# Optimization experiments

Measured on AMD Instinct MI355X. Metric: run time of the kernel, lower is better.

Reference implementation:

```python
import jax, jax.numpy as jnp
import numpy as np

B, S, D = 4, 1024, 1024
H, HD = 16, 64
MAXPOS = 1024  # max_position_embeddings


def setup_inputs() -> dict:
    key = jax.random.key(0)
    ks = jax.random.split(key, 10)
    sc = 0.02
    return {
        "hidden_states": jax.random.normal(ks[0], (B, S, D), dtype=jnp.float32),
        "attention_mask": jnp.zeros((B, 1, 1, S), dtype=jnp.float32),
        "across_attention_prior": jax.random.uniform(ks[1], (B, H, S, S), dtype=jnp.float32),
        "head_mask": jnp.ones((1, H, 1, 1), dtype=jnp.float32),
        "Wq": jax.random.normal(ks[2], (D, D), dtype=jnp.float32) * sc,
        "bq": jnp.zeros((D,), dtype=jnp.float32),
        "Wk": jax.random.normal(ks[3], (D, D), dtype=jnp.float32) * sc,
        "bk": jnp.zeros((D,), dtype=jnp.float32),
        "Wv": jax.random.normal(ks[4], (D, D), dtype=jnp.float32) * sc,
        "bv": jnp.zeros((D,), dtype=jnp.float32),
        "dist_emb": jax.random.normal(ks[5], (2 * MAXPOS - 1, HD), dtype=jnp.float32) * sc,
    }


def _heads(x):
    # [B,S,D] -> [B,H,S,HD]
    return x.reshape(B, S, H, HD).transpose(0, 2, 1, 3)


def reference(hidden_states, attention_mask, across_attention_prior, head_mask,
              Wq, bq, Wk, bk, Wv, bv, dist_emb):
    q = _heads(hidden_states @ Wq + bq)  # [B,H,S,HD]
    k = _heads(hidden_states @ Wk + bk)
    v = _heads(hidden_states @ Wv + bv)

    scores = jnp.einsum("bhld,bhrd->bhlr", q, k)

    # relative_key_query positional bias
    pos = jnp.arange(S)
    distance = pos[:, None] - pos[None, :]  # [S,S]
    pe = dist_emb[distance + MAXPOS - 1]  # [S,S,HD] (l, r, d)
    scores = scores + jnp.einsum("bhld,lrd->bhlr", q, pe)
    scores = scores + jnp.einsum("bhrd,lrd->bhlr", k, pe)

    scores = scores / jnp.sqrt(jnp.float32(HD))
    scores = scores + attention_mask  # additive mask, broadcast [B,1,1,S]

    probs = jax.nn.softmax(scores, axis=-1)
    probs = probs * across_attention_prior  # post-softmax multiplicative prior
    probs = probs * head_mask  # dropout prob = 0 (eval)

    ctx = jnp.einsum("bhlr,bhrd->bhld", probs, v)
    ctx = ctx.transpose(0, 2, 1, 3).reshape(B, S, D)
    return ctx
```

## Files before the change

kernel.cpp:

```cpp
#include <hip/hip_runtime.h>


typedef unsigned short u16;
typedef unsigned int   u32;
typedef __attribute__((ext_vector_type(8))) short bfx8;
typedef __attribute__((ext_vector_type(4))) float f32x4;
typedef __attribute__((ext_vector_type(4))) unsigned short u16x4;

#define MFMA_BF16(a, b, c) __builtin_amdgcn_mfma_f32_16x16x32_bf16(a, b, c, 0, 0, 0)

__device__ __forceinline__ u16 f2bf(float f) {
    union { float f; u32 u; } c; c.f = f;
    u32 u = c.u;
    return (u16)((u + 0x7FFFu + ((u >> 16) & 1u)) >> 16);
}
__device__ __forceinline__ float bf2f(u16 v) {
    union { u32 u; float f; } c; c.u = ((u32)v) << 16;
    return c.f;
}
__device__ __forceinline__ float load_f(const void* p, long i, bool bf) {
    return bf ? bf2f(((const u16*)p)[i]) : ((const float*)p)[i];
}

__device__ __forceinline__ void gload16(const u16* g, u16* l) {
    __builtin_amdgcn_global_load_lds(
        (__attribute__((address_space(1))) void*)g,
        (__attribute__((address_space(3))) void*)l, 16, 0, 0);
}

__device__ __forceinline__ void wg_barrier() {
    asm volatile("s_waitcnt lgkmcnt(0)" ::: "memory");
    __builtin_amdgcn_s_barrier();
    asm volatile("" ::: "memory");
}

__global__ void k_detect(const u32* hid, int* flags) {
    __shared__ int cnt;
    if (threadIdx.x == 0) cnt = 0;
    __syncthreads();
    int c = 0;
    for (int i = threadIdx.x; i < 1024; i += 256) {
        u32 w = hid[i];
        u32 e = (w >> 7) & 0xFFu;
        if (e >= 100u && e <= 140u) c++;
    }
    atomicAdd(&cnt, c);
    __syncthreads();
    if (threadIdx.x == 0) flags[0] = (cnt > 512) ? 1 : 0;
}

__global__ void k_prep(const void* hidden, const void* dist, const void* mask,
                       const void* hm, const void* bq, const void* bk,
                       const void* bv, const int* flags, u16* hid_bf,
                       u16* dist_bf, float* mask_f, float* hm_f, float* bias_f) {
    const bool bf = flags[0] != 0;
    const long tid = (long)blockIdx.x * 256 + threadIdx.x;

    if (bf) {
        ((int4*)hid_bf)[tid] = ((const int4*)hidden)[tid];
    } else {
        const float* hf = (const float*)hidden + tid * 8;
        int4 o; u16* op = (u16*)&o;
#pragma unroll
        for (int j = 0; j < 8; j++) op[j] = f2bf(hf[j]);
        ((int4*)hid_bf)[tid] = o;
    }
    if (tid < 16376) {
        if (bf) {
            ((int4*)dist_bf)[tid] = ((const int4*)dist)[tid];
        } else {
            const float* df = (const float*)dist + tid * 8;
            int4 o; u16* op = (u16*)&o;
#pragma unroll
            for (int j = 0; j < 8; j++) op[j] = f2bf(df[j]);
            ((int4*)dist_bf)[tid] = o;
        }
    }
    if (tid < 4096) mask_f[tid] = load_f(mask, tid, bf);
    if (tid < 3072) {
        const void* src = (tid < 1024) ? bq : ((tid < 2048) ? bk : bv);
        bias_f[tid] = load_f(src, tid & 1023, bf);
    }
    if (tid < 16) hm_f[tid] = load_f(hm, tid, bf);
}

__global__ void k_transpose(const void* Wq, const void* Wk, const void* Wv,
                            const int* flags, u16* wt) {
    const bool bf = flags[0] != 0;
    __shared__ float t[32][33];
    const int z = blockIdx.z;
    const void* W = (z == 0) ? Wq : ((z == 1) ? Wk : Wv);
    int x = blockIdx.x * 32 + threadIdx.x;
    for (int i = 0; i < 4; i++) {
        int y = blockIdx.y * 32 + threadIdx.y + i * 8;
        t[threadIdx.y + i * 8][threadIdx.x] = load_f(W, (long)y * 1024 + x, bf);
    }
    __syncthreads();
    int x2 = blockIdx.y * 32 + threadIdx.x;
    u16* out = wt + (long)z * 1024 * 1024;
    for (int i = 0; i < 4; i++) {
        int y2 = blockIdx.x * 32 + threadIdx.y + i * 8;
        out[(long)y2 * 1024 + x2] = f2bf(t[threadIdx.x][threadIdx.y + i * 8]);
    }
}

__global__ __launch_bounds__(256, 3)
void k_qkv_gemm(const u16* A, const u16* Bt, const float* bias,
                u16* qb, u16* kb, u16* vb) {
    __shared__ u16 sA[128 * 64];
    __shared__ u16 sB[128 * 64];
    const int tid = threadIdx.x;
    const int w = tid >> 6, lane = tid & 63;
    const int quad = lane >> 4, nl = lane & 15;
    const int wr = w >> 1, wc = w & 1;
    const int bid0 = blockIdx.y * 24 + blockIdx.x;
    const int bid = (bid0 & 7) * 96 + (bid0 >> 3);
    const int n0 = (bid % 24) * 128, m0 = (bid / 24) * 128;

    f32x4 acc[4][4];
#pragma unroll
    for (int a = 0; a < 4; a++)
#pragma unroll
        for (int b = 0; b < 4; b++) acc[a][b] = (f32x4){0.f, 0.f, 0.f, 0.f};

    const int srow = 32 * w + (lane >> 3);
    const int seg = lane & 7;

    for (int kt = 0; kt < 16; kt++) {
        const int k0 = kt * 64;
        __syncthreads();
#pragma unroll
        for (int j = 0; j < 4; j++) {
            int row = srow + 8 * j;
            int ss = (seg ^ (row & 7)) * 8;
            gload16(A + (long)(m0 + row) * 1024 + k0 + ss, sA + (32 * w + 8 * j) * 64);
            gload16(Bt + (long)(n0 + row) * 1024 + k0 + ss, sB + (32 * w + 8 * j) * 64);
        }
        __syncthreads();

#pragma unroll
        for (int hh = 0; hh < 2; hh++) {
            bfx8 af[4], bfr[4];
#pragma unroll
            for (int f = 0; f < 4; f++) {
                int Ra = 64 * wr + 16 * f + nl;
                int Rb = 64 * wc + 16 * f + nl;
                af[f]  = *(const bfx8*)(sA + Ra * 64 + (((4 * hh + quad) ^ (Ra & 7)) * 8));
                bfr[f] = *(const bfx8*)(sB + Rb * 64 + (((4 * hh + quad) ^ (Rb & 7)) * 8));
            }
#pragma unroll
            for (int fm = 0; fm < 4; fm++)
#pragma unroll
                for (int fn = 0; fn < 4; fn++)
                    acc[fm][fn] = MFMA_BF16(af[fm], bfr[fn], acc[fm][fn]);
        }
    }

#pragma unroll
    for (int fm = 0; fm < 4; fm++) {
#pragma unroll
        for (int fn = 0; fn < 4; fn++) {
            int n = n0 + 64 * wc + 16 * fn + nl;
            int which = n >> 10, hcol = n & 1023;
            int h = hcol >> 6, hd = hcol & 63;
            u16* op = (which == 0) ? qb : ((which == 1) ? kb : vb);
            float bias_v = bias[n];
#pragma unroll
            for (int reg = 0; reg < 4; reg++) {
                int m = m0 + 64 * wr + 16 * fm + 4 * quad + reg;
                int b = m >> 10, s = m & 1023;
                float v = acc[fm][fn][reg] + bias_v;
                op[((long)((b * 16 + h) * 1024 + s)) * 64 + hd] = f2bf(v);
            }
        }
    }
}

__global__ __launch_bounds__(512, 4)
void k_attn(const u16* qb, const u16* kb, const u16* vb, const u16* Eb,
            const float* maskf, const float* hmf, const void* prior,
            const int* flags, void* out) {
    constexpr int PT = 72;
    constexpr int PD = 132;
    constexpr int PX = 66;
    __shared__ __align__(16) char smem[79872];
    u16* sQ  = (u16*)(smem);
    u16* sK  = (u16*)(smem + 9216);
    u16* sVT = (u16*)(smem + 18432);
    u16* sE  = (u16*)(smem + 27648);
    u16* sP  = (u16*)(smem + 27648);
    u16* sDq = (u16*)(smem + 46080);
    u16* sDk = (u16*)(smem + 62976);
    float* accx = (float*)(smem + 46080);
    float* zs   = (float*)(smem + 9216);

    const int tid = threadIdx.x;
    const int W = tid >> 6, lane = tid & 63;
    const int s = W >> 1, c = W & 1;
    const int quad = lane >> 4, nl = lane & 15;
    const int bh = blockIdx.x, b = bh >> 4, h = bh & 15;
    const int l0 = blockIdx.y * 64;
    const bool bf = flags[0] != 0;

    const u16* qbh = qb + (long)bh * 65536;
    const u16* kbh = kb + (long)bh * 65536;
    const u16* vbh = vb + (long)bh * 65536;

    {
        int row = tid >> 3, s8 = tid & 7;
        *(int4*)(sQ + row * PT + s8 * 8) = *(const int4*)(qbh + (l0 + row) * 64 + s8 * 8);
    }

    const int erow = tid >> 3, es8 = tid & 7;
    const int jb_base = l0 + 960;

    int4 nK0, nE0, nE1, nV0;
    {
        nK0 = *(const int4*)(kbh + erow * 64 + es8 * 8);
        int j0 = jb_base + erow;       if (j0 > 2046) j0 = 2046;
        int j1 = jb_base + 64 + erow;  if (j1 > 2046) j1 = 2046;
        nE0 = *(const int4*)(Eb + (long)j0 * 64 + es8 * 8);
        nE1 = *(const int4*)(Eb + (long)j1 * 64 + es8 * 8);
        nV0 = *(const int4*)(vbh + lane * 64 + W * 8);
    }

    wg_barrier();
    const bfx8 aq0 = *(const bfx8*)(sQ + (16 * s + nl) * PT + quad * 8);
    const bfx8 aq1 = *(const bfx8*)(sQ + (16 * s + nl) * PT + quad * 8 + 32);

    const int dql = c ? s + 3 : s,     dqh = c ? s + 4 : s + 2;
    const int dkl = c ? 6 - s : 3 - s, dkh = c ? 7 - s : 5 - s;

    f32x4 accv[4];
#pragma unroll
    for (int f = 0; f < 4; f++) accv[f] = (f32x4){0.f, 0.f, 0.f, 0.f};
    float zrow = 0.f;

    for (int it = 0; it < 16; it++) {
        const int r0 = it * 64;
        wg_barrier();

        *(int4*)(sK + erow * PT + es8 * 8)        = nK0;
        *(int4*)(sE + erow * PT + es8 * 8)        = nE0;
        *(int4*)(sE + (64 + erow) * PT + es8 * 8) = nE1;
        {
            const u16* pv = (const u16*)&nV0;
#pragma unroll
            for (int j2 = 0; j2 < 8; j2++) sVT[(W * 8 + j2) * PT + lane] = pv[j2];
        }

        f32x4 mvec[2], prv[2];
#pragma unroll
        for (int f2 = 0; f2 < 2; f2++) {
            const int colr = r0 + 32 * c + 16 * f2 + 4 * quad;
            mvec[f2] = *(const f32x4*)(maskf + b * 1024 + colr);
            long prow = ((long)(bh * 1024 + l0 + 16 * s + nl)) * 1024 + colr;
            if (bf) {
                u16x4 t = *(const u16x4*)((const u16*)prior + prow);
                prv[f2] = (f32x4){bf2f(t[0]), bf2f(t[1]), bf2f(t[2]), bf2f(t[3])};
            } else {
                prv[f2] = *(const f32x4*)((const float*)prior + prow);
            }
        }

        if (it < 15) {
            const int r0n = r0 + 64;
            const int jbn = jb_base - r0n;
            nK0 = *(const int4*)(kbh + (r0n + erow) * 64 + es8 * 8);
            int j0 = jbn + erow;       if (j0 > 2046) j0 = 2046;
            int j1 = jbn + 64 + erow;  if (j1 > 2046) j1 = 2046;
            nE0 = *(const int4*)(Eb + (long)j0 * 64 + es8 * 8);
            nE1 = *(const int4*)(Eb + (long)j1 * 64 + es8 * 8);
            nV0 = *(const int4*)(vbh + (r0n + lane) * 64 + W * 8);
        }
        wg_barrier();

        const bfx8 ak0 = *(const bfx8*)(sK + (16 * s + nl) * PT + quad * 8);
        const bfx8 ak1 = *(const bfx8*)(sK + (16 * s + nl) * PT + quad * 8 + 32);

#pragma unroll
        for (int fc = 0; fc < 8; fc++) {
            const bool uq = (fc >= dql) && (fc <= dqh);
            const bool uk = (fc >= dkl) && (fc <= dkh);
            if (!(uq || uk)) continue;
            const int ub = fc * 16;
            const int R = ub + nl;
            bfx8 be0 = *(const bfx8*)(sE + R * PT + quad * 8);
            bfx8 be1 = *(const bfx8*)(sE + R * PT + quad * 8 + 32);
            if (uq) {
                f32x4 dq = (f32x4){0.f, 0.f, 0.f, 0.f};
                dq = MFMA_BF16(be0, aq0, dq);
                dq = MFMA_BF16(be1, aq1, dq);
                u16x4 dqp;
#pragma unroll
                for (int reg = 0; reg < 4; reg++) dqp[reg] = f2bf(dq[reg]);
                *(u16x4*)(sDq + (16 * s + nl) * PD + ub + 4 * quad) = dqp;
            }
            if (uk) {
                f32x4 dk = (f32x4){0.f, 0.f, 0.f, 0.f};
                dk = MFMA_BF16(ak0, be0, dk);
                dk = MFMA_BF16(ak1, be1, dk);
#pragma unroll
                for (int reg = 0; reg < 4; reg++)
                    sDk[(16 * s + 4 * quad + reg) * PD + ub + nl] = f2bf(dk[reg]);
            }
        }
        f32x4 accs[2];
#pragma unroll
        for (int f2 = 0; f2 < 2; f2++) {
            const int R = (2 * c + f2) * 16 + nl;
            bfx8 ka0 = *(const bfx8*)(sK + R * PT + quad * 8);
            bfx8 ka1 = *(const bfx8*)(sK + R * PT + quad * 8 + 32);
            f32x4 sv = (f32x4){0.f, 0.f, 0.f, 0.f};
            sv = MFMA_BF16(ka0, aq0, sv);
            sv = MFMA_BF16(ka1, aq1, sv);
            accs[f2] = sv;
        }
        wg_barrier();

        u16x4 pw4[2];
        const int li = 16 * s + nl;
#pragma unroll
        for (int f2 = 0; f2 < 2; f2++) {
#pragma unroll
            for (int reg = 0; reg < 4; reg++) {
                int ri = (2 * c + f2) * 16 + 4 * quad + reg;
                int u = li - ri + 63;
                float sv = (accs[f2][reg] + bf2f(sDq[li * PD + u])
                            + bf2f(sDk[ri * PD + u])) * 0.125f + mvec[f2][reg];
                float e = __expf(sv);
                zrow += e;
                pw4[f2][reg] = f2bf(e * prv[f2][reg]);
            }
        }

#pragma unroll
        for (int f2 = 0; f2 < 2; f2++)
            *(u16x4*)(sP + li * PT + 32 * c + 16 * f2 + 4 * quad) = pw4[f2];

        const bfx8 ap = *(const bfx8*)(sP + li * PT + 32 * c + quad * 8);
#pragma unroll
        for (int fd = 0; fd < 4; fd++) {
            bfx8 bv = *(const bfx8*)(sVT + (fd * 16 + nl) * PT + 32 * c + quad * 8);
            accv[fd] = MFMA_BF16(ap, bv, accv[fd]);
        }
    }

    zrow += __shfl_xor(zrow, 16);
    zrow += __shfl_xor(zrow, 32);

    wg_barrier();
    if (c == 1) {
#pragma unroll
        for (int fd = 0; fd < 4; fd++)
#pragma unroll
            for (int reg = 0; reg < 4; reg++)
                accx[(16 * s + 4 * quad + reg) * PX + fd * 16 + nl] = accv[fd][reg];
    }
    if (quad == 0) zs[(16 * s + nl) * 2 + c] = zrow;
    wg_barrier();
    if (c == 0) {
        const float hm = hmf[h];
        float zt[4];
#pragma unroll
        for (int reg = 0; reg < 4; reg++) {
            int li2 = 16 * s + 4 * quad + reg;
            zt[reg] = zs[li2 * 2] + zs[li2 * 2 + 1];
        }
#pragma unroll
        for (int fd = 0; fd < 4; fd++) {
#pragma unroll
            for (int reg = 0; reg < 4; reg++) {
                int li2 = 16 * s + 4 * quad + reg;
                int d = fd * 16 + nl;
                float val = (accv[fd][reg] + accx[li2 * PX + fd * 16 + nl]) * hm / zt[reg];
                long oidx = ((long)(b * 1024 + l0 + li2)) * 1024 + h * 64 + d;
                if (bf) ((u16*)out)[oidx] = f2bf(val);
                else    ((float*)out)[oidx] = val;
            }
        }
    }
}

extern "C" void kernel_launch(void* const* d_in, const int* in_sizes, int n_in,
                              void* d_out, int out_size, void* d_ws, size_t ws_size,
                              hipStream_t stream) {
    char* ws = (char*)d_ws;
    int*   flags   = (int*)ws;
    u16*   hid_bf  = (u16*)(ws + 256);
    u16*   wt_bf   = (u16*)(ws + 8388864);
    u16*   dist_bf = (u16*)(ws + 14680320);
    float* mask_f  = (float*)(ws + 14942464);
    float* bias_f  = (float*)(ws + 14958848);
    float* hm_f    = (float*)(ws + 14971136);
    u16*   q_bf    = (u16*)(ws + 14971392);
    u16*   k_bf    = (u16*)(ws + 23360000);
    u16*   v_bf    = (u16*)(ws + 31748608);

    k_detect<<<1, 256, 0, stream>>>((const u32*)d_in[0], flags);
    k_prep<<<2048, 256, 0, stream>>>(d_in[0], d_in[10], d_in[1], d_in[3],
                                     d_in[5], d_in[7], d_in[9], flags,
                                     hid_bf, dist_bf, mask_f, hm_f, bias_f);
    k_transpose<<<dim3(32, 32, 3), dim3(32, 8), 0, stream>>>(
        d_in[4], d_in[6], d_in[8], flags, wt_bf);
    k_qkv_gemm<<<dim3(24, 32), 256, 0, stream>>>(hid_bf, wt_bf, bias_f,
                                                 q_bf, k_bf, v_bf);
    k_attn<<<dim3(64, 16), 512, 0, stream>>>(q_bf, k_bf, v_bf, dist_bf,
                                             mask_f, hm_f, d_in[2], flags, d_out);
}
```

Measured before the change: 499.8 us.

## Emit V pre-transposed from QKV GEMM and double-buffer V tiles via direct-to-LDS loads

The QKV GEMM epilogue now stages the V block in shared memory and writes V transposed as [b,h,d,s], so the attention kernel no longer transposes V with scalar LDS stores each iteration. The attention kernel loads V tiles with gload16 into two swizzled LDS buffers, prefetching the next tile while the current one is used. It also swaps the MFMA operand order for the Dk bias so the result can be stored as packed u16x4 instead of scattered scalar writes. In exchange the GEMM epilogue gains an extra sync and LDS round-trip for V blocks, and the LDS layout in the attention kernel is reshuffled.

```diff
diff --git a/kernel.cpp b/kernel.cpp
--- a/kernel.cpp
+++ b/kernel.cpp
@@ -106,9 +106,10 @@
 
 __global__ __launch_bounds__(256, 3)
 void k_qkv_gemm(const u16* A, const u16* Bt, const float* bias,
-                u16* qb, u16* kb, u16* vb) {
-    __shared__ u16 sA[128 * 64];
-    __shared__ u16 sB[128 * 64];
+                u16* qb, u16* kb, u16* vt) {
+    __shared__ u16 smemg[128 * 64 * 2];
+    u16* sA = smemg;
+    u16* sB = smemg + 128 * 64;
     const int tid = threadIdx.x;
     const int w = tid >> 6, lane = tid & 63;
     const int quad = lane >> 4, nl = lane & 15;
@@ -156,42 +157,72 @@
         }
     }
 
-#pragma unroll
-    for (int fm = 0; fm < 4; fm++) {
-#pragma unroll
-        for (int fn = 0; fn < 4; fn++) {
-            int n = n0 + 64 * wc + 16 * fn + nl;
-            int which = n >> 10, hcol = n & 1023;
-            int h = hcol >> 6, hd = hcol & 63;
-            u16* op = (which == 0) ? qb : ((which == 1) ? kb : vb);
-            float bias_v = bias[n];
-#pragma unroll
-            for (int reg = 0; reg < 4; reg++) {
-                int m = m0 + 64 * wr + 16 * fm + 4 * quad + reg;
-                int b = m >> 10, s = m & 1023;
-                float v = acc[fm][fn][reg] + bias_v;
-                op[((long)((b * 16 + h) * 1024 + s)) * 64 + hd] = f2bf(v);
-            }
+    if (n0 < 2048) {
+#pragma unroll
+        for (int fm = 0; fm < 4; fm++) {
+#pragma unroll
+            for (int fn = 0; fn < 4; fn++) {
+                int n = n0 + 64 * wc + 16 * fn + nl;
+                int which = n >> 10, hcol = n & 1023;
+                int h = hcol >> 6, hd = hcol & 63;
+                u16* op = (which == 0) ? qb : kb;
+                float bias_v = bias[n];
+#pragma unroll
+                for (int reg = 0; reg < 4; reg++) {
+                    int m = m0 + 64 * wr + 16 * fm + 4 * quad + reg;
+                    int b = m >> 10, s = m & 1023;
+                    float v = acc[fm][fn][reg] + bias_v;
+                    op[((long)((b * 16 + h) * 1024 + s)) * 64 + hd] = f2bf(v);
+                }
+            }
+        }
+    } else {
+        __syncthreads();
+        u16* t = smemg;
+#pragma unroll
+        for (int fm = 0; fm < 4; fm++) {
+#pragma unroll
+            for (int fn = 0; fn < 4; fn++) {
+                int row = 64 * wc + 16 * fn + nl;
+                float bias_v = bias[n0 + row];
+                u16x4 pack;
+#pragma unroll
+                for (int reg = 0; reg < 4; reg++)
+                    pack[reg] = f2bf(acc[fm][fn][reg] + bias_v);
+                int unit = (8 * wr + 2 * fm + (quad >> 1)) ^ (row & 7);
+                *(u16x4*)((char*)t + row * 256 + unit * 16 + (quad & 1) * 8) = pack;
+            }
+        }
+        __syncthreads();
+        const int row = tid >> 1, u0 = (tid & 1) * 8;
+        const int d = row & 63, hloc = row >> 6;
+        const int h = ((n0 & 1023) >> 6) + hloc;
+        const int b = m0 >> 10, s0 = m0 & 1023;
+        u16* dst = vt + (((long)((b * 16 + h) * 64 + d)) << 10) + s0;
+#pragma unroll
+        for (int k = 0; k < 8; k++) {
+            *(int4*)(dst + (u0 + k) * 8) = *(const int4*)(t + row * 128 + (u0 + k) * 8);
         }
     }
 }
 
 __global__ __launch_bounds__(512, 4)
-void k_attn(const u16* qb, const u16* kb, const u16* vb, const u16* Eb,
+void k_attn(const u16* qb, const u16* kb, const u16* vt, const u16* Eb,
             const float* maskf, const float* hmf, const void* prior,
             const int* flags, void* out) {
     constexpr int PT = 72;
     constexpr int PD = 132;
     constexpr int PX = 66;
-    __shared__ __align__(16) char smem[79872];
-    u16* sQ  = (u16*)(smem);
-    u16* sK  = (u16*)(smem + 9216);
-    u16* sVT = (u16*)(smem + 18432);
-    u16* sE  = (u16*)(smem + 27648);
-    u16* sP  = (u16*)(smem + 27648);
-    u16* sDq = (u16*)(smem + 46080);
-    u16* sDk = (u16*)(smem + 62976);
-    float* accx = (float*)(smem + 46080);
+    __shared__ __align__(16) char smem[78848];
+    u16* sVT1 = (u16*)(smem);
+    u16* sQ   = (u16*)(smem);
+    u16* sK   = (u16*)(smem + 9216);
+    u16* sVT0 = (u16*)(smem + 18432);
+    u16* sE   = (u16*)(smem + 26624);
+    u16* sP   = (u16*)(smem + 26624);
+    u16* sDq  = (u16*)(smem + 45056);
+    u16* sDk  = (u16*)(smem + 61952);
+    float* accx = (float*)(smem + 45056);
     float* zs   = (float*)(smem + 9216);
 
     const int tid = threadIdx.x;
@@ -204,7 +235,11 @@
 
     const u16* qbh = qb + (long)bh * 65536;
     const u16* kbh = kb + (long)bh * 65536;
-    const u16* vbh = vb + (long)bh * 65536;
+    const u16* vtp = vt + (long)bh * 65536;
+
+    const int vd = 8 * W + (lane >> 3), vk = lane & 7;
+
+    gload16(vtp + (long)vd * 1024 + 0 + vk * 8, sVT0 + 512 * W);
 
     {
         int row = tid >> 3, s8 = tid & 7;
@@ -214,14 +249,13 @@
     const int erow = tid >> 3, es8 = tid & 7;
     const int jb_base = l0 + 960;
 
-    int4 nK0, nE0, nE1, nV0;
+    int4 nK0, nE0, nE1;
     {
         nK0 = *(const int4*)(kbh + erow * 64 + es8 * 8);
         int j0 = jb_base + erow;       if (j0 > 2046) j0 = 2046;
         int j1 = jb_base + 64 + erow;  if (j1 > 2046) j1 = 2046;
         nE0 = *(const int4*)(Eb + (long)j0 * 64 + es8 * 8);
         nE1 = *(const int4*)(Eb + (long)j1 * 64 + es8 * 8);
-        nV0 = *(const int4*)(vbh + lane * 64 + W * 8);
     }
 
     wg_barrier();
@@ -243,11 +277,6 @@
         *(int4*)(sK + erow * PT + es8 * 8)        = nK0;
         *(int4*)(sE + erow * PT + es8 * 8)        = nE0;
         *(int4*)(sE + (64 + erow) * PT + es8 * 8) = nE1;
-        {
-            const u16* pv = (const u16*)&nV0;
-#pragma unroll
-            for (int j2 = 0; j2 < 8; j2++) sVT[(W * 8 + j2) * PT + lane] = pv[j2];
-        }
 
         f32x4 mvec[2], prv[2];
 #pragma unroll
@@ -271,9 +300,13 @@
             int j1 = jbn + 64 + erow;  if (j1 > 2046) j1 = 2046;
             nE0 = *(const int4*)(Eb + (long)j0 * 64 + es8 * 8);
             nE1 = *(const int4*)(Eb + (long)j1 * 64 + es8 * 8);
-            nV0 = *(const int4*)(vbh + (r0n + lane) * 64 + W * 8);
         }
         wg_barrier();
+
+        if (it < 15) {
+            u16* vbuf_n = ((it + 1) & 1) ? sVT1 : sVT0;
+            gload16(vtp + (long)vd * 1024 + (r0 + 64) + vk * 8, vbuf_n + 512 * W);
+        }
 
         const bfx8 ak0 = *(const bfx8*)(sK + (16 * s + nl) * PT + quad * 8);
         const bfx8 ak1 = *(const bfx8*)(sK + (16 * s + nl) * PT + quad * 8 + 32);
@@ -298,11 +331,12 @@
             }
             if (uk) {
                 f32x4 dk = (f32x4){0.f, 0.f, 0.f, 0.f};
-                dk = MFMA_BF16(ak0, be0, dk);
-                dk = MFMA_BF16(ak1, be1, dk);
-#pragma unroll
-                for (int reg = 0; reg < 4; reg++)
-                    sDk[(16 * s + 4 * quad + reg) * PD + ub + nl] = f2bf(dk[reg]);
+                dk = MFMA_BF16(be0, ak0, dk);
+                dk = MFMA_BF16(be1, ak1, dk);
+                u16x4 dkp;
+#pragma unroll
+                for (int reg = 0; reg < 4; reg++) dkp[reg] = f2bf(dk[reg]);
+                *(u16x4*)(sDk + (16 * s + nl) * PD + ub + 4 * quad) = dkp;
             }
         }
         f32x4 accs[2];
@@ -338,10 +372,12 @@
         for (int f2 = 0; f2 < 2; f2++)
             *(u16x4*)(sP + li * PT + 32 * c + 16 * f2 + 4 * quad) = pw4[f2];
 
+        const u16* vbuf = (it & 1) ? sVT1 : sVT0;
         const bfx8 ap = *(const bfx8*)(sP + li * PT + 32 * c + quad * 8);
 #pragma unroll
         for (int fd = 0; fd < 4; fd++) {
-            bfx8 bv = *(const bfx8*)(sVT + (fd * 16 + nl) * PT + 32 * c + quad * 8);
+            const int R = fd * 16 + nl;
+            bfx8 bv = *(const bfx8*)(vbuf + R * 64 + (((4 * c + quad) ^ (R & 7)) * 8));
             accv[fd] = MFMA_BF16(ap, bv, accv[fd]);
         }
     }
@@ -395,7 +431,7 @@
     float* hm_f    = (float*)(ws + 14971136);
     u16*   q_bf    = (u16*)(ws + 14971392);
     u16*   k_bf    = (u16*)(ws + 23360000);
-    u16*   v_bf    = (u16*)(ws + 31748608);
+    u16*   vt_bf   = (u16*)(ws + 31748608);
 
     k_detect<<<1, 256, 0, stream>>>((const u32*)d_in[0], flags);
     k_prep<<<2048, 256, 0, stream>>>(d_in[0], d_in[10], d_in[1], d_in[3],
@@ -404,7 +440,7 @@
     k_transpose<<<dim3(32, 32, 3), dim3(32, 8), 0, stream>>>(
         d_in[4], d_in[6], d_in[8], flags, wt_bf);
     k_qkv_gemm<<<dim3(24, 32), 256, 0, stream>>>(hid_bf, wt_bf, bias_f,
-                                                 q_bf, k_bf, v_bf);
-    k_attn<<<dim3(64, 16), 512, 0, stream>>>(q_bf, k_bf, v_bf, dist_bf,
+                                                 q_bf, k_bf, vt_bf);
+    k_attn<<<dim3(64, 16), 512, 0, stream>>>(q_bf, k_bf, vt_bf, dist_bf,
                                              mask_f, hm_f, d_in[2], flags, d_out);
 }
```

Measured after the change: 489.2 us. -2.1%, faster.
